# Performance work log

Hardware: AMD Instinct MI355X
Metric: run time of the kernel (lower is better)

## Reference

```python
import jax, jax.numpy as jnp
from jax import lax
import numpy as np

D_MODEL = 512
D_PROJ = 256
PATCH = 4
NL = 8
D_STATE = 16
D_CONV = 4
EXPAND = 2
D_INNER = EXPAND * D_MODEL          # 1024
DT_RANK = (D_MODEL + 15) // 16      # 32
B = 4
SEQ = 1024
NF = 1
EPS = 1e-5


def setup_inputs() -> dict:
    key = jax.random.key(0)
    ks = jax.random.split(key, 12)
    s = 0.02
    def rn(k, shape):
        return jax.random.normal(k, shape, jnp.float32) * s
    A_init = jnp.log(jnp.arange(1, D_STATE + 1, dtype=jnp.float32))  # (n,)
    return {
        "time_series": jax.random.normal(ks[0], (B, SEQ, NF), jnp.float32),
        "mask": jnp.ones((B, SEQ), jnp.int32),
        "emb_w": rn(ks[1], (D_MODEL, PATCH)),
        "emb_b": jnp.zeros((D_MODEL,), jnp.float32),
        "norm_w": jnp.ones((NL, D_MODEL), jnp.float32),
        "in_w": rn(ks[2], (NL, 2, 2 * D_INNER, D_MODEL)),
        "conv_w": rn(ks[3], (NL, 2, D_INNER, D_CONV)),
        "conv_b": jnp.zeros((NL, 2, D_INNER), jnp.float32),
        "xproj_w": rn(ks[4], (NL, 2, DT_RANK + 2 * D_STATE, D_INNER)),
        "dt_w": rn(ks[5], (NL, 2, D_INNER, DT_RANK)),
        "dt_b": jnp.full((NL, 2, D_INNER), float(np.log(np.expm1(0.01))), jnp.float32),
        "A_log": jnp.broadcast_to(A_init, (NL, 2, D_INNER, D_STATE)) + jnp.zeros((NL, 2, D_INNER, D_STATE), jnp.float32),
        "Dp": jnp.ones((NL, 2, D_INNER), jnp.float32),
        "out_w": rn(ks[6], (NL, 2, D_MODEL, D_INNER)),
        "proj_w": rn(ks[7], (PATCH * D_PROJ, D_MODEL)),
        "proj_b": jnp.zeros((PATCH * D_PROJ,), jnp.float32),
    }


def rmsnorm(x, w):
    return x * lax.rsqrt(jnp.mean(x * x, axis=-1, keepdims=True) + EPS) * w


def mamba(x, in_w, conv_w, conv_b, xproj_w, dt_w, dt_b, A_log, Dp, out_w):
    # x: (B, L, D_MODEL)
    Bsz, L, _ = x.shape
    xz = jnp.einsum('bld,ed->ble', x, in_w)                 # (B,L,2*d_inner)
    u, z = jnp.split(xz, 2, axis=-1)                         # each (B,L,d_inner)
    # depthwise causal conv1d along L
    u_t = jnp.transpose(u, (0, 2, 1))                        # (B,d_inner,L)
    u_pad = jnp.pad(u_t, ((0, 0), (0, 0), (D_CONV - 1, 0)))
    conv = lax.conv_general_dilated(
        u_pad, conv_w[:, None, :], window_strides=(1,), padding='VALID',
        feature_group_count=D_INNER, dimension_numbers=('NCH', 'OIH', 'NCH'))
    u = jax.nn.silu(jnp.transpose(conv + conv_b[None, :, None], (0, 2, 1)))  # (B,L,d_inner)
    x_dbl = jnp.einsum('ble,re->blr', u, xproj_w)            # (B,L,dt_rank+2n)
    dt, Bm, C = jnp.split(x_dbl, [DT_RANK, DT_RANK + D_STATE], axis=-1)
    delta = jax.nn.softplus(jnp.einsum('blr,er->ble', dt, dt_w) + dt_b)  # (B,L,d_inner)
    A = -jnp.exp(A_log)                                      # (d_inner,n)

    def step(h, inp):
        d_t, B_t, C_t, u_t = inp                             # (B,e),(B,n),(B,n),(B,e)
        dA = jnp.exp(d_t[..., None] * A)                     # (B,e,n)
        h = dA * h + (d_t * u_t)[..., None] * B_t[:, None, :]
        y = jnp.einsum('ben,bn->be', h, C_t)
        return h, y

    h0 = jnp.zeros((Bsz, D_INNER, D_STATE), x.dtype)
    xs = (jnp.moveaxis(delta, 1, 0), jnp.moveaxis(Bm, 1, 0),
          jnp.moveaxis(C, 1, 0), jnp.moveaxis(u, 1, 0))
    _, ys = lax.scan(step, h0, xs)                           # ys: (L,B,e)
    y = jnp.moveaxis(ys, 0, 1) + u * Dp
    y = y * jax.nn.silu(z)
    return jnp.einsum('ble,de->bld', y, out_w)               # (B,L,D_MODEL)


def reference(time_series, mask, emb_w, emb_b, norm_w, in_w, conv_w, conv_b,
              xproj_w, dt_w, dt_b, A_log, Dp, out_w, proj_w, proj_b):
    Bsz, S, F_ = time_series.shape
    NP = S // PATCH  # S is a multiple of PATCH
    patches = time_series.reshape(Bsz, NP, PATCH, F_)
    patches = jnp.transpose(patches, (0, 3, 1, 2)).reshape(Bsz, F_ * NP, PATCH)
    x = patches @ emb_w.T + emb_b                            # (B, F*NP, D_MODEL)
    for i in range(NL):
        res = x
        xn = rmsnorm(x, norm_w[i])
        yf = mamba(xn, in_w[i, 0], conv_w[i, 0], conv_b[i, 0], xproj_w[i, 0],
                   dt_w[i, 0], dt_b[i, 0], A_log[i, 0], Dp[i, 0], out_w[i, 0])
        yb = mamba(jnp.flip(xn, axis=1), in_w[i, 1], conv_w[i, 1], conv_b[i, 1],
                   xproj_w[i, 1], dt_w[i, 1], dt_b[i, 1], A_log[i, 1], Dp[i, 1], out_w[i, 1])
        x = yf + jnp.flip(yb, axis=1) + res
    proj = x @ proj_w.T + proj_b                             # (B, F*NP, PATCH*D_PROJ)
    le = proj.reshape(Bsz, F_, NP, PATCH, D_PROJ)
    le = jnp.transpose(le, (0, 2, 3, 1, 4)).reshape(Bsz, NP * PATCH, F_, D_PROJ)
    return le[:, :S]
```

## Files before the change

### kernel.cpp

```cpp
#include <hip/hip_runtime.h>
#include <hip/hip_bf16.h>

#define DM 512
#define DI 1024
#define DSTATE 16
#define DTR 32
#define NLAYER 8
#define BS 4
#define LL 256
#define MT 1024
#define DPROJ 256

typedef unsigned short u16;
typedef unsigned int u32;
typedef __attribute__((ext_vector_type(8))) short short8;
typedef __attribute__((ext_vector_type(4))) float f32x4;

__device__ __forceinline__ float sigmoidf_(float x){ return 1.f/(1.f+__expf(-x)); }

__device__ __forceinline__ u16 f2bf(float f){
  unsigned u = __float_as_uint(f);
  u = (u + 0x7FFF + ((u>>16)&1)) >> 16;
  return (u16)u;
}
__device__ __forceinline__ float bf2f(u16 v){
  return __uint_as_float(((unsigned)v) << 16);
}

template<int CTRL>
__device__ __forceinline__ float dpp_ror_add(float x){
  int y = __builtin_amdgcn_update_dpp(0, __float_as_int(x), CTRL, 0xF, 0xF, false);
  return x + __int_as_float(y);
}
__device__ __forceinline__ float sum16_dpp(float x){
  x = dpp_ror_add<0x128>(x);
  x = dpp_ror_add<0x124>(x);
  x = dpp_ror_add<0x122>(x);
  x = dpp_ror_add<0x121>(x);
  return x;
}

__global__ __launch_bounds__(256) void embed_k(const float* __restrict__ ts,
    const float* __restrict__ ew, const float* __restrict__ eb, float* __restrict__ x){
  int idx = blockIdx.x*256 + threadIdx.x;
  int m = idx >> 9, d = idx & 511;
  int b = m >> 8, np_ = m & 255;
  const float* t0 = ts + b*1024 + np_*4;
  float acc = eb[d];
  #pragma unroll
  for (int p=0;p<4;p++) acc = fmaf(t0[p], ew[d*4+p], acc);
  x[idx] = acc;
}

__global__ __launch_bounds__(256) void wcastall_k(
    const float* __restrict__ w_in, const float* __restrict__ w_out,
    const float* __restrict__ w_xp, const float* __restrict__ w_pj,
    u16* __restrict__ dst){
  int t = blockIdx.x*256 + threadIdx.x;
  long e4 = (long)t*4;
  const float* src; long o;
  if      (e4 < 16777216) { src = w_in;  o = e4; }
  else if (e4 < 25165824) { src = w_out; o = e4 - 16777216; }
  else if (e4 < 26214400) { src = w_xp;  o = e4 - 25165824; }
  else                    { src = w_pj;  o = e4 - 26214400; }
  float4 v = *(const float4*)(src + o);
  ushort4 r; r.x=f2bf(v.x); r.y=f2bf(v.y); r.z=f2bf(v.z); r.w=f2bf(v.w);
  *(ushort4*)(dst + e4) = r;
}

__global__ __launch_bounds__(256) void rmscomb_k(float* __restrict__ x,
    const float* __restrict__ yout,
    const float* __restrict__ nw, u16* __restrict__ xnbf, u16* __restrict__ xnfbf){
  int m = blockIdx.x, t = threadIdx.x;
  int b = m>>8, l = m&255, mf = (b<<8)+(255-l);
  float2 v = *(const float2*)&x[(long)m*DM + t*2];
  if (yout){
    float2 f = *(const float2*)&yout[(long)m*DM + t*2];
    float2 g = *(const float2*)&yout[(long)MT*DM + (long)mf*DM + t*2];
    v.x += f.x + g.x; v.y += f.y + g.y;
    *(float2*)&x[(long)m*DM + t*2] = v;
  }
  float ss = v.x*v.x + v.y*v.y;
  ss += __shfl_down(ss,32); ss += __shfl_down(ss,16); ss += __shfl_down(ss,8);
  ss += __shfl_down(ss,4);  ss += __shfl_down(ss,2);  ss += __shfl_down(ss,1);
  __shared__ float ps[4];
  if ((t&63)==0) ps[t>>6] = ss;
  __syncthreads();
  float tot = ps[0]+ps[1]+ps[2]+ps[3];
  float rs = rsqrtf(tot*(1.f/DM) + 1e-5f);
  ushort2 o; o.x = f2bf(v.x*rs*nw[t*2]); o.y = f2bf(v.y*rs*nw[t*2+1]);
  *(ushort2*)&xnbf [(long)m *DM + t*2] = o;
  *(ushort2*)&xnfbf[(long)mf*DM + t*2] = o;
}

__global__ __launch_bounds__(256) void combcast_k(const float* __restrict__ x,
    const float* __restrict__ yout, u16* __restrict__ xbf){
  int idx = blockIdx.x*256 + threadIdx.x;
  int m = idx >> 7, c4 = idx & 127;
  int b = m>>8, l = m&255, mf = (b<<8)+(255-l);
  float4 r = ((const float4*)x)[idx];
  float4 f = ((const float4*)yout)[idx];
  float4 g = ((const float4*)(yout + (long)MT*DM))[(long)mf*128 + c4];
  ushort4 o;
  o.x = f2bf(r.x + f.x + g.x); o.y = f2bf(r.y + f.y + g.y);
  o.z = f2bf(r.z + f.z + g.z); o.w = f2bf(r.w + f.w + g.w);
  ((ushort4*)xbf)[idx] = o;
}

template<int BM,int BN,int SPLITK,int EPI>
__global__ __launch_bounds__(256) void mfma_nt(
    const u16* __restrict__ A, int lda, long sA,
    const u16* __restrict__ W, int ldw, long sW,
    const float* __restrict__ bias, u16* __restrict__ G,
    float* __restrict__ C, int ldc, long sC,
    int M, int N, int K)
{
  constexpr int WM = BM/2, WN = BN/2;
  constexpr int MI = WM/16, NI = WN/16;
  int z = blockIdx.z;
  int dir = z / SPLITK, kc = z % SPLITK;
  int Klen = K / SPLITK;
  int kbase = kc * Klen;
  A += (long)dir * sA;
  W += (long)dir * sW;
  if (SPLITK > 1) C += (long)z * M * N; else C += (long)dir * sC;
  if (EPI==4) G += (long)dir * (long)MT*DI;

  __shared__ u16 Al[BM*32];
  __shared__ u16 Wl[BN*32];
  int tid = threadIdx.x;
  int lane = tid & 63;
  int wave = tid >> 6;
  int wm0 = (wave>>1)*WM, wn0 = (wave&1)*WN;
  int m0 = blockIdx.y*BM, n0 = blockIdx.x*BN;
  int l16 = lane>>4, l15 = lane&15;

  f32x4 acc[MI][NI] = {};

  for (int k0=0; k0<Klen; k0+=32){
    #pragma unroll
    for (int it=0; it<BM*4/256; ++it){
      int ch = it*256 + tid;
      int row = ch % BM, kk = ch / BM;
      const u16* g = A + (long)(m0+row)*lda + kbase + k0 + kk*8;
      __builtin_amdgcn_global_load_lds(
          (const __attribute__((address_space(1))) void*)g,
          (__attribute__((address_space(3))) void*)(Al + ch*8), 16, 0, 0);
    }
    #pragma unroll
    for (int it=0; it<BN*4/256; ++it){
      int ch = it*256 + tid;
      int row = ch % BN, kk = ch / BN;
      const u16* g = W + (long)(n0+row)*ldw + kbase + k0 + kk*8;
      __builtin_amdgcn_global_load_lds(
          (const __attribute__((address_space(1))) void*)g,
          (__attribute__((address_space(3))) void*)(Wl + ch*8), 16, 0, 0);
    }
    __syncthreads();
    short8 a[MI], b[NI];
    #pragma unroll
    for (int i=0;i<MI;i++)
      a[i] = *(const short8*)&Al[(l16*BM + wm0 + i*16 + l15)*8];
    #pragma unroll
    for (int j=0;j<NI;j++)
      b[j] = *(const short8*)&Wl[(l16*BN + wn0 + j*16 + l15)*8];
    #pragma unroll
    for (int i=0;i<MI;i++)
      #pragma unroll
      for (int j=0;j<NI;j++)
        acc[i][j] = __builtin_amdgcn_mfma_f32_16x16x32_bf16(a[i], b[j], acc[i][j], 0,0,0);
    __syncthreads();
  }
  #pragma unroll
  for (int i=0;i<MI;i++){
    #pragma unroll
    for (int j=0;j<NI;j++){
      #pragma unroll
      for (int r=0;r<4;r++){
        int m = m0 + wm0 + i*16 + l16*4 + r;
        int n = n0 + wn0 + j*16 + l15;
        float v = acc[i][j][r];
        if (EPI==2){
          v += bias[n];
          int bb = m>>8, np_ = m&255, p = n>>8, dp = n&255;
          C[((long)(bb*1024 + np_*4 + p))*256 + dp] = v;
        } else if (EPI==4){
          if (n < 1024) C[(long)m*1024 + n] = v;
          else          G[(long)m*1024 + (n-1024)] = f2bf(v * sigmoidf_(v));
        } else {
          C[(long)m*ldc + n] = v;
        }
      }
    }
  }
}

__global__ __launch_bounds__(256) void xreduce_k(const float* __restrict__ part,
    float* __restrict__ xdbl){
  int idx = blockIdx.x*256 + threadIdx.x;
  int d = idx >> 16, off = idx & 65535;
  float s = 0.f;
  #pragma unroll
  for (int kc=0; kc<8; ++kc) s += part[((d*8+kc)<<16) + off];
  xdbl[idx] = s;
}

__global__ __launch_bounds__(256) void conv_silu_k(const float* __restrict__ xzu,
    const float* __restrict__ cw, const float* __restrict__ cb,
    u16* __restrict__ ubf){
  int idx = blockIdx.x*256 + threadIdx.x;
  int e = idx & (DI-1);
  int grp = idx >> 10;
  int dir = grp >> 8;
  int b   = (grp >> 6) & 3;
  int l0  = (grp & 63) * 4;
  long dm0 = (long)dir*MT + b*LL + l0;
  const float* w = cw + ((long)dir*DI + e)*4;
  float w0=w[0], w1=w[1], w2=w[2], w3=w[3];
  float bias = cb[dir*DI + e];
  const float* src = xzu + dm0*DI + e;
  float vb[7];
  #pragma unroll
  for (int j=0;j<7;j++){
    int l = l0 - 3 + j;
    vb[j] = (l >= 0) ? src[(long)(j-3)*DI] : 0.f;
  }
  #pragma unroll
  for (int j=0;j<4;j++){
    float acc = bias;
    acc = fmaf(w0, vb[j],   acc);
    acc = fmaf(w1, vb[j+1], acc);
    acc = fmaf(w2, vb[j+2], acc);
    acc = fmaf(w3, vb[j+3], acc);
    float v = acc * sigmoidf_(acc);
    ubf[(dm0+j)*DI + e] = f2bf(v);
  }
}

__global__ __launch_bounds__(64) void scan_k(
    const u16* __restrict__ ubf, const u16* __restrict__ gbf,
    const float* __restrict__ xdbl, const float* __restrict__ dtw,
    const float* __restrict__ dtb, const float* __restrict__ A_log,
    const float* __restrict__ Dp, u16* __restrict__ ygbf)
{
  int t = threadIdx.x;
  int n = t & 15, g = t >> 4;
  int id = blockIdx.x + 256*blockIdx.y + 1024*blockIdx.z;
  int xcd = id & 7, s = id >> 3;
  int ecb = xcd*32 + (s & 31);
  int rest = s >> 5;
  int b = rest & 3, dir = rest >> 2;
  int e0 = ecb*4;

  long mbase = (long)dir*MT + b*LL;
  const u16* up_ = ubf + mbase*DI + e0;
  const u16* gp_ = gbf + mbase*DI + e0;
  const float* xd_ = xdbl + mbase*64;
  u16* yp_ = ygbf + mbase*DI + e0;

  float Av = -__expf(A_log[((long)dir*DI + e0 + g)*16 + n]);
  float Dv = Dp[dir*DI + e0 + g];

  float wrow[32];
  {
    const float* wr = dtw + ((long)dir*DI + e0 + g)*32;
    #pragma unroll
    for (int r4=0;r4<8;r4++) *(float4*)&wrow[r4*4] = *(const float4*)&wr[r4*4];
  }
  float dtbv = dtb[dir*DI + e0 + g];

  __shared__ u32 sDU[4][80];
  __shared__ u32 sBC[16][36];
  __shared__ float sy[32][4];

  ushort4 ru, rg;
  float4 rb0, rb1, rc0, rc1;
  int brow = t >> 1, bseg = t & 1;

  auto loadrg = [&](int c){
    int l0 = c*32;
    if (t < 32){
      ru = *(const ushort4*)&up_[(long)(l0 + t)*DI];
      rg = *(const ushort4*)&gp_[(long)(l0 + t)*DI];
    }
    const float* src = &xd_[(long)(l0 + brow)*64 + 32 + bseg*8];
    rb0 = *(const float4*)&src[0];
    rb1 = *(const float4*)&src[4];
    rc0 = *(const float4*)&src[16];
    rc1 = *(const float4*)&src[20];
  };

  loadrg(0);
  float h = 0.f;

  for (int c = 0; c < 8; ++c){
    int l0 = c*32;
    if (t < 32){
      sDU[0][2*t+1] = ru.x; sDU[1][2*t+1] = ru.y;
      sDU[2][2*t+1] = ru.z; sDU[3][2*t+1] = ru.w;
    }
    {
      u32 pb[8];
      pb[0] = (u32)f2bf(rb0.x) | ((u32)f2bf(rc0.x)<<16);
      pb[1] = (u32)f2bf(rb0.y) | ((u32)f2bf(rc0.y)<<16);
      pb[2] = (u32)f2bf(rb0.z) | ((u32)f2bf(rc0.z)<<16);
      pb[3] = (u32)f2bf(rb0.w) | ((u32)f2bf(rc0.w)<<16);
      pb[4] = (u32)f2bf(rb1.x) | ((u32)f2bf(rc1.x)<<16);
      pb[5] = (u32)f2bf(rb1.y) | ((u32)f2bf(rc1.y)<<16);
      pb[6] = (u32)f2bf(rb1.z) | ((u32)f2bf(rc1.z)<<16);
      pb[7] = (u32)f2bf(rb1.w) | ((u32)f2bf(rc1.w)<<16);
      #pragma unroll
      for (int k=0;k<8;k++) sBC[bseg*8 + k][brow] = pb[k];
    }
    #pragma unroll
    for (int j=0;j<2;j++){
      int l = n + j*16;
      const float* row = &xd_[(long)(l0 + l)*64];
      float acc = dtbv;
      #pragma unroll
      for (int r4=0;r4<8;r4++){
        float4 d4 = *(const float4*)&row[r4*4];
        acc = fmaf(d4.x, wrow[r4*4],   acc);
        acc = fmaf(d4.y, wrow[r4*4+1], acc);
        acc = fmaf(d4.z, wrow[r4*4+2], acc);
        acc = fmaf(d4.w, wrow[r4*4+3], acc);
      }
      acc = fmaxf(acc, 0.f) + __logf(1.f + __expf(-fabsf(acc)));
      sDU[g][2*l] = __float_as_uint(acc);
    }
    ushort4 gcur = rg;
    __syncthreads();
    if (c < 7) loadrg(c+1);

    float dA[32], sv[32], ud[32];
    u32  bcp[32];
    {
      const u32* pdu = &sDU[g][0];
      const u32* pbc = &sBC[n][0];
      #pragma unroll
      for (int l4=0; l4<8; ++l4){
        uint4 a0 = *(const uint4*)&pdu[l4*8];
        uint4 a1 = *(const uint4*)&pdu[l4*8+4];
        uint4 bc = *(const uint4*)&pbc[l4*4];
        int L = l4*4;
        float dv0 = __uint_as_float(a0.x), uv0 = bf2f((u16)a0.y);
        float dv1 = __uint_as_float(a0.z), uv1 = bf2f((u16)a0.w);
        float dv2 = __uint_as_float(a1.x), uv2 = bf2f((u16)a1.y);
        float dv3 = __uint_as_float(a1.z), uv3 = bf2f((u16)a1.w);
        dA[L  ] = __expf(dv0*Av); sv[L  ] = dv0*uv0*bf2f((u16)(bc.x & 0xffff)); ud[L  ] = uv0*Dv;
        dA[L+1] = __expf(dv1*Av); sv[L+1] = dv1*uv1*bf2f((u16)(bc.y & 0xffff)); ud[L+1] = uv1*Dv;
        dA[L+2] = __expf(dv2*Av); sv[L+2] = dv2*uv2*bf2f((u16)(bc.z & 0xffff)); ud[L+2] = uv2*Dv;
        dA[L+3] = __expf(dv3*Av); sv[L+3] = dv3*uv3*bf2f((u16)(bc.w & 0xffff)); ud[L+3] = uv3*Dv;
        bcp[L] = bc.x; bcp[L+1] = bc.y; bcp[L+2] = bc.z; bcp[L+3] = bc.w;
      }
    }
    #pragma unroll
    for (int l=0; l<32; ++l){
      h = fmaf(dA[l], h, sv[l]);
      sv[l] = h;
    }
    #pragma unroll
    for (int l=0; l<32; ++l) sv[l] *= bf2f((u16)(bcp[l] >> 16));
    #pragma unroll
    for (int l=0; l<32; ++l) sv[l] = sum16_dpp(sv[l]);
    if (n == 0){
      #pragma unroll
      for (int l=0; l<32; ++l) sy[l][g] = sv[l] + ud[l];
    }
    __builtin_amdgcn_wave_barrier();

    if (t < 32){
      float4 y4 = *(const float4*)&sy[t][0];
      ushort4 o;
      o.x = f2bf(y4.x * bf2f(gcur.x)); o.y = f2bf(y4.y * bf2f(gcur.y));
      o.z = f2bf(y4.z * bf2f(gcur.z)); o.w = f2bf(y4.w * bf2f(gcur.w));
      *(ushort4*)&yp_[(long)(l0 + t)*DI] = o;
    }
    __syncthreads();
  }
}

extern "C" void kernel_launch(void* const* d_in, const int* in_sizes, int n_in,
                              void* d_out, int out_size, void* d_ws, size_t ws_size,
                              hipStream_t stream){
  const float* ts   = (const float*)d_in[0];
  const float* ew   = (const float*)d_in[2];
  const float* eb   = (const float*)d_in[3];
  const float* nw   = (const float*)d_in[4];
  const float* inw  = (const float*)d_in[5];
  const float* cw   = (const float*)d_in[6];
  const float* cb   = (const float*)d_in[7];
  const float* xpw  = (const float*)d_in[8];
  const float* dtw  = (const float*)d_in[9];
  const float* dtb  = (const float*)d_in[10];
  const float* alog = (const float*)d_in[11];
  const float* dpp  = (const float*)d_in[12];
  const float* outw = (const float*)d_in[13];
  const float* pw   = (const float*)d_in[14];
  const float* pb   = (const float*)d_in[15];
  float* out = (float*)d_out;

  float* ws   = (float*)d_ws;
  float* x    = ws;
  float* xzu  = ws + 524288;
  float* xdbl = ws + 2621440;
  float* yout = ws + 2752512;
  float* xpart= ws + 3801088;
  u16* ub     = (u16*)(ws + 4849664);
  u16* xn_bf  = ub;
  u16* u_bf   = ub + 1048576;
  u16* g_bf   = ub + 3145728;
  u16* yg_bf  = ub + 5242880;
  u16* x_bf   = ub + 7340032;
  u16* wb     = ub + 7864320;
  u16* wb_in  = wb;
  u16* wb_out = wb + 16777216;
  u16* wb_xp  = wb + 25165824;
  u16* wb_pj  = wb + 26214400;

  dim3 blk(256);

  embed_k<<<MT*DM/256, blk, 0, stream>>>(ts, ew, eb, x);
  wcastall_k<<<26112, blk, 0, stream>>>(inw, outw, xpw, pw, wb);

  for (int i=0;i<NLAYER;i++){
    rmscomb_k<<<MT, blk, 0, stream>>>(x, i ? yout : nullptr, nw + i*DM,
        xn_bf, xn_bf + MT*DM);
    mfma_nt<64,128,1,4><<<dim3(16,16,2), blk, 0, stream>>>(
        xn_bf, DM, (long)MT*DM, wb_in + (long)i*2097152, DM, 1048576,
        nullptr, g_bf, xzu, 1024, (long)MT*1024, MT, 2048, DM);
    conv_silu_k<<<2048, blk, 0, stream>>>(xzu, cw + (long)i*2*DI*4, cb + i*2*DI, u_bf);
    mfma_nt<64,64,8,0><<<dim3(1,16,16), blk, 0, stream>>>(
        u_bf, DI, (long)MT*DI, wb_xp + (long)i*131072, DI, 65536,
        nullptr, nullptr, xpart, 64, 0, MT, 64, DI);
    xreduce_k<<<512, blk, 0, stream>>>(xpart, xdbl);
    scan_k<<<dim3(256, BS, 2), dim3(64), 0, stream>>>(u_bf, g_bf, xdbl,
        dtw + (long)i*2*DI*DTR, dtb + (long)i*2*DI,
        alog + (long)i*2*DI*16, dpp + i*2*DI, yg_bf);
    mfma_nt<64,64,1,0><<<dim3(8,16,2), blk, 0, stream>>>(
        yg_bf, DI, (long)MT*DI, wb_out + (long)i*1048576, DI, 524288,
        nullptr, nullptr, yout, DM, (long)MT*DM, MT, DM, DI);
  }
  combcast_k<<<MT*DM/4/256, blk, 0, stream>>>(x, yout, x_bf);
  mfma_nt<64,64,1,2><<<dim3(16,16,1), blk, 0, stream>>>(
      x_bf, DM, 0, wb_pj, DM, 0, pb, nullptr, out, 1024, 0, MT, 1024, DM);
}
```

Measured before the change: 824.6 us.

## Remap scan blocks to 2 channels x 2 batches per wave; halve weight-cast grid

The selective-scan kernel now gives each 64-thread block 2 inner channels for 2 batch sequences, instead of 4 channels for one batch. Every thread now does the global loads, where before only half did, and each half-wave reads its own B/C rows directly with wider per-thread loads. Shared-memory buffers gain a sequence dimension. The weight-cast kernel processes two float4 chunks per thread with half the blocks, which adds per-thread work in exchange for fewer block launches.

Result: slower. 911.5 us (+10.5%).

```diff
diff --git a/kernel.cpp b/kernel.cpp
--- a/kernel.cpp
+++ b/kernel.cpp
@@ -52,20 +52,25 @@
   x[idx] = acc;
 }
 
+#define WTOT 6684672
+#define WHALF 3342336
 __global__ __launch_bounds__(256) void wcastall_k(
     const float* __restrict__ w_in, const float* __restrict__ w_out,
     const float* __restrict__ w_xp, const float* __restrict__ w_pj,
     u16* __restrict__ dst){
   int t = blockIdx.x*256 + threadIdx.x;
-  long e4 = (long)t*4;
-  const float* src; long o;
-  if      (e4 < 16777216) { src = w_in;  o = e4; }
-  else if (e4 < 25165824) { src = w_out; o = e4 - 16777216; }
-  else if (e4 < 26214400) { src = w_xp;  o = e4 - 25165824; }
-  else                    { src = w_pj;  o = e4 - 26214400; }
-  float4 v = *(const float4*)(src + o);
-  ushort4 r; r.x=f2bf(v.x); r.y=f2bf(v.y); r.z=f2bf(v.z); r.w=f2bf(v.w);
-  *(ushort4*)(dst + e4) = r;
+  #pragma unroll
+  for (int hh=0; hh<2; ++hh){
+    long e4 = ((long)t + (long)hh*WHALF)*4;
+    const float* src; long o;
+    if      (e4 < 16777216) { src = w_in;  o = e4; }
+    else if (e4 < 25165824) { src = w_out; o = e4 - 16777216; }
+    else if (e4 < 26214400) { src = w_xp;  o = e4 - 25165824; }
+    else                    { src = w_pj;  o = e4 - 26214400; }
+    float4 v = *(const float4*)(src + o);
+    ushort4 r; r.x=f2bf(v.x); r.y=f2bf(v.y); r.z=f2bf(v.z); r.w=f2bf(v.w);
+    *(ushort4*)(dst + e4) = r;
+  }
 }
 
 __global__ __launch_bounds__(256) void rmscomb_k(float* __restrict__ x,
@@ -244,13 +249,16 @@
     const float* __restrict__ Dp, u16* __restrict__ ygbf)
 {
   int t = threadIdx.x;
-  int n = t & 15, g = t >> 4;
-  int id = blockIdx.x + 256*blockIdx.y + 1024*blockIdx.z;
+  int n = t & 15;
+  int g = (t >> 4) & 1;
+  int sq = t >> 5;
+  int id = blockIdx.x + 512*blockIdx.y + 1024*blockIdx.z;
   int xcd = id & 7, s = id >> 3;
-  int ecb = xcd*32 + (s & 31);
-  int rest = s >> 5;
-  int b = rest & 3, dir = rest >> 2;
-  int e0 = ecb*4;
+  int ecb = xcd*64 + (s & 63);
+  int rest = s >> 6;
+  int bp = rest & 1, dir = rest >> 1;
+  int e0 = ecb*2;
+  int b = bp*2 + sq;
 
   long mbase = (long)dir*MT + b*LL;
   const u16* up_ = ubf + mbase*DI + e0;
@@ -269,25 +277,21 @@
   }
   float dtbv = dtb[dir*DI + e0 + g];
 
-  __shared__ u32 sDU[4][80];
-  __shared__ u32 sBC[16][36];
-  __shared__ float sy[32][4];
-
-  ushort4 ru, rg;
-  float4 rb0, rb1, rc0, rc1;
-  int brow = t >> 1, bseg = t & 1;
+  __shared__ u32 sDU[2][2][80];
+  __shared__ u32 sBC[2][16][36];
+  __shared__ float sy[2][32][2];
+
+  int idx32 = t & 31;
+  u32 ru, rg;
+  float4 rbc[8];
 
   auto loadrg = [&](int c){
     int l0 = c*32;
-    if (t < 32){
-      ru = *(const ushort4*)&up_[(long)(l0 + t)*DI];
-      rg = *(const ushort4*)&gp_[(long)(l0 + t)*DI];
-    }
-    const float* src = &xd_[(long)(l0 + brow)*64 + 32 + bseg*8];
-    rb0 = *(const float4*)&src[0];
-    rb1 = *(const float4*)&src[4];
-    rc0 = *(const float4*)&src[16];
-    rc1 = *(const float4*)&src[20];
+    ru = *(const u32*)&up_[(long)(l0 + idx32)*DI];
+    rg = *(const u32*)&gp_[(long)(l0 + idx32)*DI];
+    const float* src = &xd_[(long)(l0 + idx32)*64 + 32];
+    #pragma unroll
+    for (int j=0;j<8;j++) rbc[j] = *(const float4*)&src[j*4];
   };
 
   loadrg(0);
@@ -295,22 +299,18 @@
 
   for (int c = 0; c < 8; ++c){
     int l0 = c*32;
-    if (t < 32){
-      sDU[0][2*t+1] = ru.x; sDU[1][2*t+1] = ru.y;
-      sDU[2][2*t+1] = ru.z; sDU[3][2*t+1] = ru.w;
-    }
+    sDU[sq][0][2*idx32+1] = (u32)(ru & 0xffff);
+    sDU[sq][1][2*idx32+1] = (u32)(ru >> 16);
     {
-      u32 pb[8];
-      pb[0] = (u32)f2bf(rb0.x) | ((u32)f2bf(rc0.x)<<16);
-      pb[1] = (u32)f2bf(rb0.y) | ((u32)f2bf(rc0.y)<<16);
-      pb[2] = (u32)f2bf(rb0.z) | ((u32)f2bf(rc0.z)<<16);
-      pb[3] = (u32)f2bf(rb0.w) | ((u32)f2bf(rc0.w)<<16);
-      pb[4] = (u32)f2bf(rb1.x) | ((u32)f2bf(rc1.x)<<16);
-      pb[5] = (u32)f2bf(rb1.y) | ((u32)f2bf(rc1.y)<<16);
-      pb[6] = (u32)f2bf(rb1.z) | ((u32)f2bf(rc1.z)<<16);
-      pb[7] = (u32)f2bf(rb1.w) | ((u32)f2bf(rc1.w)<<16);
-      #pragma unroll
-      for (int k=0;k<8;k++) sBC[bseg*8 + k][brow] = pb[k];
+      #pragma unroll
+      for (int j=0;j<4;j++){
+        float4 Bq = rbc[j];
+        float4 Cq = rbc[j+4];
+        sBC[sq][4*j  ][idx32] = (u32)f2bf(Bq.x) | ((u32)f2bf(Cq.x)<<16);
+        sBC[sq][4*j+1][idx32] = (u32)f2bf(Bq.y) | ((u32)f2bf(Cq.y)<<16);
+        sBC[sq][4*j+2][idx32] = (u32)f2bf(Bq.z) | ((u32)f2bf(Cq.z)<<16);
+        sBC[sq][4*j+3][idx32] = (u32)f2bf(Bq.w) | ((u32)f2bf(Cq.w)<<16);
+      }
     }
     #pragma unroll
     for (int j=0;j<2;j++){
@@ -326,17 +326,17 @@
         acc = fmaf(d4.w, wrow[r4*4+3], acc);
       }
       acc = fmaxf(acc, 0.f) + __logf(1.f + __expf(-fabsf(acc)));
-      sDU[g][2*l] = __float_as_uint(acc);
-    }
-    ushort4 gcur = rg;
+      sDU[sq][g][2*l] = __float_as_uint(acc);
+    }
+    u32 gcur = rg;
     __syncthreads();
     if (c < 7) loadrg(c+1);
 
     float dA[32], sv[32], ud[32];
     u32  bcp[32];
     {
-      const u32* pdu = &sDU[g][0];
-      const u32* pbc = &sBC[n][0];
+      const u32* pdu = &sDU[sq][g][0];
+      const u32* pbc = &sBC[sq][n][0];
       #pragma unroll
       for (int l4=0; l4<8; ++l4){
         uint4 a0 = *(const uint4*)&pdu[l4*8];
@@ -365,16 +365,15 @@
     for (int l=0; l<32; ++l) sv[l] = sum16_dpp(sv[l]);
     if (n == 0){
       #pragma unroll
-      for (int l=0; l<32; ++l) sy[l][g] = sv[l] + ud[l];
+      for (int l=0; l<32; ++l) sy[sq][l][g] = sv[l] + ud[l];
     }
     __builtin_amdgcn_wave_barrier();
 
-    if (t < 32){
-      float4 y4 = *(const float4*)&sy[t][0];
-      ushort4 o;
-      o.x = f2bf(y4.x * bf2f(gcur.x)); o.y = f2bf(y4.y * bf2f(gcur.y));
-      o.z = f2bf(y4.z * bf2f(gcur.z)); o.w = f2bf(y4.w * bf2f(gcur.w));
-      *(ushort4*)&yp_[(long)(l0 + t)*DI] = o;
+    {
+      float2 y2 = *(const float2*)&sy[sq][idx32][0];
+      u32 o = (u32)f2bf(y2.x * bf2f((u16)(gcur & 0xffff)))
+            | ((u32)f2bf(y2.y * bf2f((u16)(gcur >> 16))) << 16);
+      *(u32*)&yp_[(long)(l0 + idx32)*DI] = o;
     }
     __syncthreads();
   }
@@ -421,7 +420,7 @@
   dim3 blk(256);
 
   embed_k<<<MT*DM/256, blk, 0, stream>>>(ts, ew, eb, x);
-  wcastall_k<<<26112, blk, 0, stream>>>(inw, outw, xpw, pw, wb);
+  wcastall_k<<<13056, blk, 0, stream>>>(inw, outw, xpw, pw, wb);
 
   for (int i=0;i<NLAYER;i++){
     rmscomb_k<<<MT, blk, 0, stream>>>(x, i ? yout : nullptr, nw + i*DM,
@@ -434,7 +433,7 @@
         u_bf, DI, (long)MT*DI, wb_xp + (long)i*131072, DI, 65536,
         nullptr, nullptr, xpart, 64, 0, MT, 64, DI);
     xreduce_k<<<512, blk, 0, stream>>>(xpart, xdbl);
-    scan_k<<<dim3(256, BS, 2), dim3(64), 0, stream>>>(u_bf, g_bf, xdbl,
+    scan_k<<<dim3(512, 2, 2), dim3(64), 0, stream>>>(u_bf, g_bf, xdbl,
         dtw + (long)i*2*DI*DTR, dtb + (long)i*2*DI,
         alog + (long)i*2*DI*16, dpp + i*2*DI, yg_bf);
     mfma_nt<64,64,1,0><<<dim3(8,16,2), blk, 0, stream>>>(
```
